# Optimization experiments

Hardware: AMD Instinct MI355X
Metric: run time of the kernel (lower is better)

The kernel has to match this reference:

```python
import jax, jax.numpy as jnp
import numpy as np


def setup_inputs() -> dict:
    key = jax.random.key(0)
    kq, kk, kv = jax.random.split(key, 3)
    B, H, S, D = 2, 16, 2048, 64
    q = jax.random.normal(kq, (B, H, S, D), dtype=jnp.float32)
    k = jax.random.normal(kk, (B, H, S, D), dtype=jnp.float32)
    v = jax.random.normal(kv, (B, H, S, D), dtype=jnp.float32)
    return {"q": q, "k": k, "v": v}


def reference(q, k, v):
    # Tiled attention without online softmax computes the same math as
    # standard scaled dot-product attention (non-causal).
    D = q.shape[-1]
    scale = 1.0 / jnp.sqrt(jnp.asarray(D, dtype=q.dtype))
    # scores: [B, H, Sq, Sk]
    scores = jnp.einsum("bhqd,bhkd->bhqk", q, k) * scale
    attn = jax.nn.softmax(scores, axis=-1)
    out = jnp.einsum("bhqk,bhkd->bhqd", attn, v)
    return out
```

## Files before the change

### kernel.cpp

```cpp
#include <hip/hip_runtime.h>
#include <hip/hip_bf16.h>


#define B_ 2
#define H_ 16
#define S_ 2048
#define D_ 64
#define BH_ (B_ * H_)
#define QBLK 128
#define KVBLK 64
#define NKV (S_ / KVBLK)
#define NWAVE 8

typedef __bf16 bf16_t;
typedef bf16_t bf16x8 __attribute__((ext_vector_type(8)));
typedef bf16_t bf16x4 __attribute__((ext_vector_type(4)));
typedef float f32x4 __attribute__((ext_vector_type(4)));

__device__ __forceinline__ f32x4 mfma_16x16x32(bf16x8 a, bf16x8 b, f32x4 c) {
  return __builtin_amdgcn_mfma_f32_16x16x32_bf16(a, b, c, 0, 0, 0);
}

__device__ __forceinline__ void gload_lds16(const bf16_t* g, bf16_t* l) {
  __builtin_amdgcn_global_load_lds(
      (const __attribute__((address_space(1))) unsigned int*)g,
      (__attribute__((address_space(3))) unsigned int*)l, 16, 0, 0);
}

__global__ void convert_k_kernel(const float* __restrict__ k, bf16_t* __restrict__ kb) {
  int i = blockIdx.x * blockDim.x + threadIdx.x;
  float4 x = ((const float4*)k)[i];
  bf16x4 o = { (bf16_t)x.x, (bf16_t)x.y, (bf16_t)x.z, (bf16_t)x.w };
  *(bf16x4*)(kb + (size_t)i * 4) = o;
}

__global__ void transpose_v_kernel(const float* __restrict__ v, bf16_t* __restrict__ vt) {
  __shared__ float tile[64][65];
  int bh = blockIdx.y, kt = blockIdx.x;
  const float* vp = v + ((size_t)bh * S_ + (size_t)kt * 64) * D_;
  int r0 = threadIdx.x >> 4;
  int c4 = (threadIdx.x & 15) * 4;
#pragma unroll
  for (int p = 0; p < 4; ++p) {
    int r = r0 + p * 16;
    float4 x = *(const float4*)(vp + (size_t)r * D_ + c4);
    tile[r][c4 + 0] = x.x; tile[r][c4 + 1] = x.y;
    tile[r][c4 + 2] = x.z; tile[r][c4 + 3] = x.w;
  }
  __syncthreads();
  bf16_t* op = vt + (size_t)bh * D_ * S_ + (size_t)kt * 64;
#pragma unroll
  for (int p = 0; p < 4; ++p) {
    int d = r0 + p * 16;
    bf16x4 o = { (bf16_t)tile[c4 + 0][d], (bf16_t)tile[c4 + 1][d],
                 (bf16_t)tile[c4 + 2][d], (bf16_t)tile[c4 + 3][d] };
    *(bf16x4*)(op + (size_t)d * S_ + c4) = o;
  }
}

__global__ __launch_bounds__(512) void attn_kernel(
    const float* __restrict__ q, const bf16_t* __restrict__ kb,
    const bf16_t* __restrict__ vt, float* __restrict__ out) {
  const int bh = blockIdx.y;
  const int qt = blockIdx.x;
  const int tid = threadIdx.x;
  const int wid = tid >> 6;
  const int lane = tid & 63;
  const int lr = lane & 15;
  const int lg = lane >> 4;

  __shared__ __align__(16) bf16_t ktile[2][KVBLK * D_];
  __shared__ __align__(16) bf16_t vtile[2][D_ * KVBLK];
  __shared__ __align__(16) bf16_t plds[NWAVE][16][72];

  const float* qp = q + ((size_t)bh * S_ + (size_t)qt * QBLK + wid * 16) * D_;
  const bf16_t* kp = kb + (size_t)bh * S_ * D_;
  const bf16_t* vp = vt + (size_t)bh * D_ * S_;

  const int srow = tid >> 3;
  const int sc = (tid & 7) ^ (srow & 7);
  const int ksrc = srow * D_ + sc * 8;
  const size_t vsrc = (size_t)srow * S_ + sc * 8;
  const int ldst = wid * 512;

  const float qscale = 0.125f * 1.4426950408889634f;
  bf16x8 bq[2];
#pragma unroll
  for (int ks = 0; ks < 2; ++ks) {
    const float* p = qp + (size_t)lr * D_ + ks * 32 + lg * 8;
    float4 x0 = *(const float4*)(p);
    float4 x1 = *(const float4*)(p + 4);
    bf16x8 a;
    a[0] = (bf16_t)(x0.x * qscale); a[1] = (bf16_t)(x0.y * qscale);
    a[2] = (bf16_t)(x0.z * qscale); a[3] = (bf16_t)(x0.w * qscale);
    a[4] = (bf16_t)(x1.x * qscale); a[5] = (bf16_t)(x1.y * qscale);
    a[6] = (bf16_t)(x1.z * qscale); a[7] = (bf16_t)(x1.w * qscale);
    bq[ks] = a;
  }

  float l = 0.f;
  f32x4 o[4];
#pragma unroll
  for (int dc = 0; dc < 4; ++dc) o[dc] = (f32x4){0.f, 0.f, 0.f, 0.f};

  gload_lds16(kp + ksrc, &ktile[0][ldst]);
  gload_lds16(vp + vsrc, &vtile[0][ldst]);
  __syncthreads();

  const int swz = lr & 7;
  const int ch_a0 = (lg ^ swz) * 8;
  const int ch_a1 = ((lg + 4) ^ swz) * 8;

  int cur = 0;
  for (int kt = 0; kt < NKV; ++kt) {
    if (kt + 1 < NKV) {
      const bf16_t* kg = kp + (size_t)(kt + 1) * (KVBLK * D_);
      const bf16_t* vg = vp + (size_t)(kt + 1) * KVBLK;
      gload_lds16(kg + ksrc, &ktile[cur ^ 1][ldst]);
      gload_lds16(vg + vsrc, &vtile[cur ^ 1][ldst]);
    }

    f32x4 s[4];
#pragma unroll
    for (int sub = 0; sub < 4; ++sub) {
      const bf16_t* krow = &ktile[cur][(sub * 16 + lr) * D_];
      bf16x8 a0 = *(const bf16x8*)(krow + ch_a0);
      bf16x8 a1 = *(const bf16x8*)(krow + ch_a1);
      f32x4 acc = (f32x4){0.f, 0.f, 0.f, 0.f};
      acc = mfma_16x16x32(a0, bq[0], acc);
      acc = mfma_16x16x32(a1, bq[1], acc);
      s[sub] = acc;
    }

    float ps = 0.f;
#pragma unroll
    for (int sub = 0; sub < 4; ++sub) {
      bf16x4 pe;
#pragma unroll
      for (int r = 0; r < 4; ++r) {
        float e = __builtin_amdgcn_exp2f(s[sub][r]);
        ps += e;
        pe[r] = (bf16_t)e;
      }
      *(bf16x4*)&plds[wid][lr][sub * 16 + lg * 4] = pe;
    }
    l += ps;

    bf16x8 pb0 = *(const bf16x8*)&plds[wid][lr][lg * 8];
    bf16x8 pb1 = *(const bf16x8*)&plds[wid][lr][32 + lg * 8];

#pragma unroll
    for (int dc = 0; dc < 4; ++dc) {
      const bf16_t* vrow = &vtile[cur][(dc * 16 + lr) * KVBLK];
      bf16x8 a0 = *(const bf16x8*)(vrow + ch_a0);
      bf16x8 a1 = *(const bf16x8*)(vrow + ch_a1);
      o[dc] = mfma_16x16x32(a0, pb0, o[dc]);
      o[dc] = mfma_16x16x32(a1, pb1, o[dc]);
    }

    __syncthreads();
    cur ^= 1;
  }

  l += __shfl_xor(l, 16, 64);
  l += __shfl_xor(l, 32, 64);
  float inv = 1.f / l;
  float* op = out + ((size_t)bh * S_ + (size_t)qt * QBLK + wid * 16 + lr) * D_;
#pragma unroll
  for (int dc = 0; dc < 4; ++dc) {
    float4 w = { o[dc][0] * inv, o[dc][1] * inv, o[dc][2] * inv, o[dc][3] * inv };
    *(float4*)(op + dc * 16 + lg * 4) = w;
  }
}

extern "C" void kernel_launch(void* const* d_in, const int* in_sizes, int n_in,
                              void* d_out, int out_size, void* d_ws, size_t ws_size,
                              hipStream_t stream) {
  const float* q = (const float*)d_in[0];
  const float* k = (const float*)d_in[1];
  const float* v = (const float*)d_in[2];
  float* out = (float*)d_out;

  bf16_t* kb = (bf16_t*)d_ws;
  bf16_t* vt = kb + (size_t)BH_ * S_ * D_;

  int n4 = (BH_ * S_ * D_) / 4;
  convert_k_kernel<<<n4 / 256, 256, 0, stream>>>(k, kb);
  transpose_v_kernel<<<dim3(S_ / 64, BH_), 256, 0, stream>>>(v, vt);
  attn_kernel<<<dim3(S_ / QBLK, BH_), 512, 0, stream>>>(q, kb, vt, out);
}
```

Before: 67.49 us.

## Process two 16-row query sub-tiles per wave with 4 waves per block

The attention kernel now runs 4 waves per block instead of 8, and each wave handles 32 query rows as two 16-row halves. Every K and V fragment read from LDS feeds two MFMAs, which halves LDS read traffic per output. Each thread issues two async global-to-LDS loads per tile to make up for having fewer threads. In exchange, register pressure rises from the doubled accumulators and Q fragments, and there are fewer waves to hide latency, though the launch bounds ask for 3 blocks per CU.

Result: slower. 76.55 us (+13.4%).

```diff
diff --git a/kernel.cpp b/kernel.cpp
--- a/kernel.cpp
+++ b/kernel.cpp
@@ -10,7 +10,7 @@
 #define QBLK 128
 #define KVBLK 64
 #define NKV (S_ / KVBLK)
-#define NWAVE 8
+#define NWAVE 4
 
 typedef __bf16 bf16_t;
 typedef bf16_t bf16x8 __attribute__((ext_vector_type(8)));
@@ -58,7 +58,7 @@
   }
 }
 
-__global__ __launch_bounds__(512) void attn_kernel(
+__global__ __launch_bounds__(256, 3) void attn_kernel(
     const float* __restrict__ q, const bf16_t* __restrict__ kb,
     const bf16_t* __restrict__ vt, float* __restrict__ out) {
   const int bh = blockIdx.y;
@@ -71,40 +71,51 @@
 
   __shared__ __align__(16) bf16_t ktile[2][KVBLK * D_];
   __shared__ __align__(16) bf16_t vtile[2][D_ * KVBLK];
-  __shared__ __align__(16) bf16_t plds[NWAVE][16][72];
-
-  const float* qp = q + ((size_t)bh * S_ + (size_t)qt * QBLK + wid * 16) * D_;
+  __shared__ __align__(16) bf16_t plds[NWAVE][32][80];
+
+  const float* qp = q + ((size_t)bh * S_ + (size_t)qt * QBLK + wid * 32) * D_;
   const bf16_t* kp = kb + (size_t)bh * S_ * D_;
   const bf16_t* vp = vt + (size_t)bh * D_ * S_;
 
-  const int srow = tid >> 3;
-  const int sc = (tid & 7) ^ (srow & 7);
-  const int ksrc = srow * D_ + sc * 8;
-  const size_t vsrc = (size_t)srow * S_ + sc * 8;
-  const int ldst = wid * 512;
+  const int p0 = wid * 128 + lane;
+  const int p1 = p0 + 64;
+  const int r0 = p0 >> 3, c0 = (p0 & 7) ^ (r0 & 7);
+  const int r1 = p1 >> 3, c1 = (p1 & 7) ^ (r1 & 7);
+  const int ks0 = r0 * D_ + c0 * 8;
+  const int ks1 = r1 * D_ + c1 * 8;
+  const size_t vs0 = (size_t)r0 * S_ + c0 * 8;
+  const size_t vs1 = (size_t)r1 * S_ + c1 * 8;
+  const int ld0 = wid * 1024;
+  const int ld1 = ld0 + 512;
 
   const float qscale = 0.125f * 1.4426950408889634f;
-  bf16x8 bq[2];
-#pragma unroll
-  for (int ks = 0; ks < 2; ++ks) {
-    const float* p = qp + (size_t)lr * D_ + ks * 32 + lg * 8;
-    float4 x0 = *(const float4*)(p);
-    float4 x1 = *(const float4*)(p + 4);
-    bf16x8 a;
-    a[0] = (bf16_t)(x0.x * qscale); a[1] = (bf16_t)(x0.y * qscale);
-    a[2] = (bf16_t)(x0.z * qscale); a[3] = (bf16_t)(x0.w * qscale);
-    a[4] = (bf16_t)(x1.x * qscale); a[5] = (bf16_t)(x1.y * qscale);
-    a[6] = (bf16_t)(x1.z * qscale); a[7] = (bf16_t)(x1.w * qscale);
-    bq[ks] = a;
-  }
-
-  float l = 0.f;
-  f32x4 o[4];
-#pragma unroll
-  for (int dc = 0; dc < 4; ++dc) o[dc] = (f32x4){0.f, 0.f, 0.f, 0.f};
-
-  gload_lds16(kp + ksrc, &ktile[0][ldst]);
-  gload_lds16(vp + vsrc, &vtile[0][ldst]);
+  bf16x8 bq[2][2];
+#pragma unroll
+  for (int qh = 0; qh < 2; ++qh)
+#pragma unroll
+    for (int ks = 0; ks < 2; ++ks) {
+      const float* p = qp + (size_t)(qh * 16 + lr) * D_ + ks * 32 + lg * 8;
+      float4 x0 = *(const float4*)(p);
+      float4 x1 = *(const float4*)(p + 4);
+      bf16x8 a;
+      a[0] = (bf16_t)(x0.x * qscale); a[1] = (bf16_t)(x0.y * qscale);
+      a[2] = (bf16_t)(x0.z * qscale); a[3] = (bf16_t)(x0.w * qscale);
+      a[4] = (bf16_t)(x1.x * qscale); a[5] = (bf16_t)(x1.y * qscale);
+      a[6] = (bf16_t)(x1.z * qscale); a[7] = (bf16_t)(x1.w * qscale);
+      bq[qh][ks] = a;
+    }
+
+  float l[2] = {0.f, 0.f};
+  f32x4 o[2][4];
+#pragma unroll
+  for (int qh = 0; qh < 2; ++qh)
+#pragma unroll
+    for (int dc = 0; dc < 4; ++dc) o[qh][dc] = (f32x4){0.f, 0.f, 0.f, 0.f};
+
+  gload_lds16(kp + ks0, &ktile[0][ld0]);
+  gload_lds16(kp + ks1, &ktile[0][ld1]);
+  gload_lds16(vp + vs0, &vtile[0][ld0]);
+  gload_lds16(vp + vs1, &vtile[0][ld1]);
   __syncthreads();
 
   const int swz = lr & 7;
@@ -116,60 +127,80 @@
     if (kt + 1 < NKV) {
       const bf16_t* kg = kp + (size_t)(kt + 1) * (KVBLK * D_);
       const bf16_t* vg = vp + (size_t)(kt + 1) * KVBLK;
-      gload_lds16(kg + ksrc, &ktile[cur ^ 1][ldst]);
-      gload_lds16(vg + vsrc, &vtile[cur ^ 1][ldst]);
-    }
-
-    f32x4 s[4];
+      gload_lds16(kg + ks0, &ktile[cur ^ 1][ld0]);
+      gload_lds16(kg + ks1, &ktile[cur ^ 1][ld1]);
+      gload_lds16(vg + vs0, &vtile[cur ^ 1][ld0]);
+      gload_lds16(vg + vs1, &vtile[cur ^ 1][ld1]);
+    }
+
+    f32x4 s[2][4];
 #pragma unroll
     for (int sub = 0; sub < 4; ++sub) {
       const bf16_t* krow = &ktile[cur][(sub * 16 + lr) * D_];
       bf16x8 a0 = *(const bf16x8*)(krow + ch_a0);
       bf16x8 a1 = *(const bf16x8*)(krow + ch_a1);
-      f32x4 acc = (f32x4){0.f, 0.f, 0.f, 0.f};
-      acc = mfma_16x16x32(a0, bq[0], acc);
-      acc = mfma_16x16x32(a1, bq[1], acc);
-      s[sub] = acc;
-    }
-
-    float ps = 0.f;
-#pragma unroll
-    for (int sub = 0; sub < 4; ++sub) {
-      bf16x4 pe;
-#pragma unroll
-      for (int r = 0; r < 4; ++r) {
-        float e = __builtin_amdgcn_exp2f(s[sub][r]);
-        ps += e;
-        pe[r] = (bf16_t)e;
+#pragma unroll
+      for (int qh = 0; qh < 2; ++qh) {
+        f32x4 acc = (f32x4){0.f, 0.f, 0.f, 0.f};
+        acc = mfma_16x16x32(a0, bq[qh][0], acc);
+        acc = mfma_16x16x32(a1, bq[qh][1], acc);
+        s[qh][sub] = acc;
       }
-      *(bf16x4*)&plds[wid][lr][sub * 16 + lg * 4] = pe;
-    }
-    l += ps;
-
-    bf16x8 pb0 = *(const bf16x8*)&plds[wid][lr][lg * 8];
-    bf16x8 pb1 = *(const bf16x8*)&plds[wid][lr][32 + lg * 8];
+    }
+
+#pragma unroll
+    for (int qh = 0; qh < 2; ++qh) {
+      float ps = 0.f;
+#pragma unroll
+      for (int sub = 0; sub < 4; ++sub) {
+        bf16x4 pe;
+#pragma unroll
+        for (int r = 0; r < 4; ++r) {
+          float e = __builtin_amdgcn_exp2f(s[qh][sub][r]);
+          ps += e;
+          pe[r] = (bf16_t)e;
+        }
+        *(bf16x4*)&plds[wid][qh * 16 + lr][sub * 16 + lg * 4] = pe;
+      }
+      l[qh] += ps;
+    }
+
+    bf16x8 pb0[2], pb1[2];
+#pragma unroll
+    for (int qh = 0; qh < 2; ++qh) {
+      pb0[qh] = *(const bf16x8*)&plds[wid][qh * 16 + lr][lg * 8];
+      pb1[qh] = *(const bf16x8*)&plds[wid][qh * 16 + lr][32 + lg * 8];
+    }
 
 #pragma unroll
     for (int dc = 0; dc < 4; ++dc) {
       const bf16_t* vrow = &vtile[cur][(dc * 16 + lr) * KVBLK];
       bf16x8 a0 = *(const bf16x8*)(vrow + ch_a0);
       bf16x8 a1 = *(const bf16x8*)(vrow + ch_a1);
-      o[dc] = mfma_16x16x32(a0, pb0, o[dc]);
-      o[dc] = mfma_16x16x32(a1, pb1, o[dc]);
+#pragma unroll
+      for (int qh = 0; qh < 2; ++qh) {
+        o[qh][dc] = mfma_16x16x32(a0, pb0[qh], o[qh][dc]);
+        o[qh][dc] = mfma_16x16x32(a1, pb1[qh], o[qh][dc]);
+      }
     }
 
     __syncthreads();
     cur ^= 1;
   }
 
-  l += __shfl_xor(l, 16, 64);
-  l += __shfl_xor(l, 32, 64);
-  float inv = 1.f / l;
-  float* op = out + ((size_t)bh * S_ + (size_t)qt * QBLK + wid * 16 + lr) * D_;
-#pragma unroll
-  for (int dc = 0; dc < 4; ++dc) {
-    float4 w = { o[dc][0] * inv, o[dc][1] * inv, o[dc][2] * inv, o[dc][3] * inv };
-    *(float4*)(op + dc * 16 + lg * 4) = w;
+#pragma unroll
+  for (int qh = 0; qh < 2; ++qh) {
+    float lq = l[qh];
+    lq += __shfl_xor(lq, 16, 64);
+    lq += __shfl_xor(lq, 32, 64);
+    float inv = 1.f / lq;
+    float* op = out + ((size_t)bh * S_ + (size_t)qt * QBLK + wid * 32 + qh * 16 + lr) * D_;
+#pragma unroll
+    for (int dc = 0; dc < 4; ++dc) {
+      float4 w = { o[qh][dc][0] * inv, o[qh][dc][1] * inv,
+                   o[qh][dc][2] * inv, o[qh][dc][3] * inv };
+      *(float4*)(op + dc * 16 + lg * 4) = w;
+    }
   }
 }
 
@@ -187,5 +218,5 @@
   int n4 = (BH_ * S_ * D_) / 4;
   convert_k_kernel<<<n4 / 256, 256, 0, stream>>>(k, kb);
   transpose_v_kernel<<<dim3(S_ / 64, BH_), 256, 0, stream>>>(v, vt);
-  attn_kernel<<<dim3(S_ / QBLK, BH_), 512, 0, stream>>>(q, kb, vt, out);
-}
+  attn_kernel<<<dim3(S_ / QBLK, BH_), 256, 0, stream>>>(q, kb, vt, out);
+}
```

## Switch attention to 32x32x16 MFMA with in-register P and split-KV waves

Applied to the files above, without the earlier changes.

Rewrites the attention kernel to use 32x32x16 bf16 MFMA tiles. Each wave now owns 32 query rows and one of two KV halves, so the block processes two KV tiles per iteration and the two partial results are combined in LDS at the end. The softmax probabilities are packed to bf16 with v_cvt_pk_bf16_f32 and rearranged with v_permlane32_swap, which removes the per-iteration LDS round trip for P. The aim is fewer MFMA issues and fewer LDS accesses per unit of work. The cost is higher register pressure, a 64KB LDS footprint, and an extra cross-wave reduction.

Result: faster. 58.87 us (-12.8%).

```diff
diff --git a/kernel.cpp b/kernel.cpp
--- a/kernel.cpp
+++ b/kernel.cpp
@@ -1,5 +1,6 @@
 #include <hip/hip_runtime.h>
 #include <hip/hip_bf16.h>
+#include <stdint.h>
 
 
 #define B_ 2
@@ -10,15 +11,26 @@
 #define QBLK 128
 #define KVBLK 64
 #define NKV (S_ / KVBLK)
-#define NWAVE 8
+#define NPER (NKV / 2)
 
 typedef __bf16 bf16_t;
 typedef bf16_t bf16x8 __attribute__((ext_vector_type(8)));
 typedef bf16_t bf16x4 __attribute__((ext_vector_type(4)));
-typedef float f32x4 __attribute__((ext_vector_type(4)));
-
-__device__ __forceinline__ f32x4 mfma_16x16x32(bf16x8 a, bf16x8 b, f32x4 c) {
-  return __builtin_amdgcn_mfma_f32_16x16x32_bf16(a, b, c, 0, 0, 0);
+typedef float f32x16 __attribute__((ext_vector_type(16)));
+typedef uint32_t u32;
+
+__device__ __forceinline__ f32x16 mfma32(bf16x8 a, bf16x8 b, f32x16 c) {
+  return __builtin_amdgcn_mfma_f32_32x32x16_bf16(a, b, c, 0, 0, 0);
+}
+
+__device__ __forceinline__ u32 cvt_pk_bf16(float lo, float hi) {
+  u32 r;
+  asm("v_cvt_pk_bf16_f32 %0, %1, %2" : "=v"(r) : "v"(lo), "v"(hi));
+  return r;
+}
+
+__device__ __forceinline__ void swap32(u32& x, u32& y) {
+  asm("v_permlane32_swap_b32 %0, %1" : "+v"(x), "+v"(y));
 }
 
 __device__ __forceinline__ void gload_lds16(const bf16_t* g, bf16_t* l) {
@@ -58,7 +70,7 @@
   }
 }
 
-__global__ __launch_bounds__(512) void attn_kernel(
+__global__ __launch_bounds__(512, 4) void attn_kernel(
     const float* __restrict__ q, const bf16_t* __restrict__ kb,
     const bf16_t* __restrict__ vt, float* __restrict__ out) {
   const int bh = blockIdx.y;
@@ -66,28 +78,32 @@
   const int tid = threadIdx.x;
   const int wid = tid >> 6;
   const int lane = tid & 63;
-  const int lr = lane & 15;
-  const int lg = lane >> 4;
-
-  __shared__ __align__(16) bf16_t ktile[2][KVBLK * D_];
-  __shared__ __align__(16) bf16_t vtile[2][D_ * KVBLK];
-  __shared__ __align__(16) bf16_t plds[NWAVE][16][72];
-
-  const float* qp = q + ((size_t)bh * S_ + (size_t)qt * QBLK + wid * 16) * D_;
+  const int wq = wid & 3;
+  const int wkv = wid >> 2;
+  const int l31 = lane & 31;
+  const int hi = lane >> 5;
+
+  __shared__ __align__(16) char smem[65536];
+  bf16_t* kbuf = (bf16_t*)smem;
+  bf16_t* vbuf = (bf16_t*)(smem + 32768);
+  float* epi = (float*)smem;
+
   const bf16_t* kp = kb + (size_t)bh * S_ * D_;
   const bf16_t* vp = vt + (size_t)bh * D_ * S_;
 
   const int srow = tid >> 3;
-  const int sc = (tid & 7) ^ (srow & 7);
-  const int ksrc = srow * D_ + sc * 8;
-  const size_t vsrc = (size_t)srow * S_ + sc * 8;
+  const int scol = (tid & 7) ^ (srow & 7);
+  const int kofs = srow * D_ + scol * 8;
+  const size_t vofs = (size_t)srow * S_ + scol * 8;
   const int ldst = wid * 512;
 
   const float qscale = 0.125f * 1.4426950408889634f;
-  bf16x8 bq[2];
-#pragma unroll
-  for (int ks = 0; ks < 2; ++ks) {
-    const float* p = qp + (size_t)lr * D_ + ks * 32 + lg * 8;
+  const int qrow = qt * QBLK + wq * 32 + l31;
+  const float* qpr = q + ((size_t)bh * S_ + qrow) * D_;
+  bf16x8 bq[4];
+#pragma unroll
+  for (int ks = 0; ks < 4; ++ks) {
+    const float* p = qpr + ks * 16 + hi * 8;
     float4 x0 = *(const float4*)(p);
     float4 x1 = *(const float4*)(p + 4);
     bf16x8 a;
@@ -98,78 +114,112 @@
     bq[ks] = a;
   }
 
-  float l = 0.f;
-  f32x4 o[4];
-#pragma unroll
-  for (int dc = 0; dc < 4; ++dc) o[dc] = (f32x4){0.f, 0.f, 0.f, 0.f};
-
-  gload_lds16(kp + ksrc, &ktile[0][ldst]);
-  gload_lds16(vp + vsrc, &vtile[0][ldst]);
+  float lsum = 0.f;
+  f32x16 o0, o1;
+#pragma unroll
+  for (int r = 0; r < 16; ++r) { o0[r] = 0.f; o1[r] = 0.f; }
+
+#pragma unroll
+  for (int par = 0; par < 2; ++par) {
+    gload_lds16(kp + (size_t)par * (KVBLK * D_) + kofs, kbuf + par * 4096 + ldst);
+    gload_lds16(vp + (size_t)par * KVBLK + vofs, vbuf + par * 4096 + ldst);
+  }
   __syncthreads();
 
-  const int swz = lr & 7;
-  const int ch_a0 = (lg ^ swz) * 8;
-  const int ch_a1 = ((lg + 4) ^ swz) * 8;
-
-  int cur = 0;
-  for (int kt = 0; kt < NKV; ++kt) {
-    if (kt + 1 < NKV) {
-      const bf16_t* kg = kp + (size_t)(kt + 1) * (KVBLK * D_);
-      const bf16_t* vg = vp + (size_t)(kt + 1) * KVBLK;
-      gload_lds16(kg + ksrc, &ktile[cur ^ 1][ldst]);
-      gload_lds16(vg + vsrc, &vtile[cur ^ 1][ldst]);
+  for (int p = 0; p < NPER; ++p) {
+    if (p + 1 < NPER) {
+      const int nb = ((p + 1) & 1) * 2;
+#pragma unroll
+      for (int par = 0; par < 2; ++par) {
+        const int t = 2 * p + 2 + par;
+        gload_lds16(kp + (size_t)t * (KVBLK * D_) + kofs,
+                    kbuf + (nb + par) * 4096 + ldst);
+        gload_lds16(vp + (size_t)t * KVBLK + vofs,
+                    vbuf + (nb + par) * 4096 + ldst);
+      }
     }
 
-    f32x4 s[4];
-#pragma unroll
-    for (int sub = 0; sub < 4; ++sub) {
-      const bf16_t* krow = &ktile[cur][(sub * 16 + lr) * D_];
-      bf16x8 a0 = *(const bf16x8*)(krow + ch_a0);
-      bf16x8 a1 = *(const bf16x8*)(krow + ch_a1);
-      f32x4 acc = (f32x4){0.f, 0.f, 0.f, 0.f};
-      acc = mfma_16x16x32(a0, bq[0], acc);
-      acc = mfma_16x16x32(a1, bq[1], acc);
-      s[sub] = acc;
+    const bf16_t* kt_ = kbuf + ((p & 1) * 2 + wkv) * 4096;
+    const bf16_t* vt_ = vbuf + ((p & 1) * 2 + wkv) * 4096;
+
+    u32 w[2][8];
+#pragma unroll
+    for (int sub = 0; sub < 2; ++sub) {
+      f32x16 sv;
+#pragma unroll
+      for (int r = 0; r < 16; ++r) sv[r] = 0.f;
+#pragma unroll
+      for (int ks = 0; ks < 4; ++ks) {
+        const int row = sub * 32 + l31;
+        const int ch = (2 * ks + hi) ^ (row & 7);
+        bf16x8 a = *(const bf16x8*)(kt_ + row * D_ + ch * 8);
+        sv = mfma32(a, bq[ks], sv);
+      }
+#pragma unroll
+      for (int b = 0; b < 4; ++b) {
+        float e0 = __builtin_amdgcn_exp2f(sv[4 * b + 0]);
+        float e1 = __builtin_amdgcn_exp2f(sv[4 * b + 1]);
+        float e2 = __builtin_amdgcn_exp2f(sv[4 * b + 2]);
+        float e3 = __builtin_amdgcn_exp2f(sv[4 * b + 3]);
+        lsum += (e0 + e1) + (e2 + e3);
+        w[sub][2 * b + 0] = cvt_pk_bf16(e0, e1);
+        w[sub][2 * b + 1] = cvt_pk_bf16(e2, e3);
+      }
+#pragma unroll
+      for (int kt2 = 0; kt2 < 2; ++kt2) {
+        swap32(w[sub][4 * kt2 + 0], w[sub][4 * kt2 + 2]);
+        swap32(w[sub][4 * kt2 + 1], w[sub][4 * kt2 + 3]);
+      }
     }
 
-    float ps = 0.f;
-#pragma unroll
-    for (int sub = 0; sub < 4; ++sub) {
-      bf16x4 pe;
-#pragma unroll
-      for (int r = 0; r < 4; ++r) {
-        float e = __builtin_amdgcn_exp2f(s[sub][r]);
-        ps += e;
-        pe[r] = (bf16_t)e;
-      }
-      *(bf16x4*)&plds[wid][lr][sub * 16 + lg * 4] = pe;
+#pragma unroll
+    for (int sub = 0; sub < 2; ++sub)
+#pragma unroll
+      for (int kt2 = 0; kt2 < 2; ++kt2) {
+        union { u32 u[4]; bf16x8 v; } pb;
+        pb.u[0] = w[sub][4 * kt2 + 0]; pb.u[1] = w[sub][4 * kt2 + 1];
+        pb.u[2] = w[sub][4 * kt2 + 2]; pb.u[3] = w[sub][4 * kt2 + 3];
+        {
+          const int row = l31;
+          const int ch = (4 * sub + 2 * kt2 + hi) ^ (row & 7);
+          bf16x8 a = *(const bf16x8*)(vt_ + row * KVBLK + ch * 8);
+          o0 = mfma32(a, pb.v, o0);
+        }
+        {
+          const int row = 32 + l31;
+          const int ch = (4 * sub + 2 * kt2 + hi) ^ (row & 7);
+          bf16x8 a = *(const bf16x8*)(vt_ + row * KVBLK + ch * 8);
+          o1 = mfma32(a, pb.v, o1);
+        }
+      }
+
+    __syncthreads();
+  }
+
+  if (wkv == 1) {
+    float* e = epi + ((size_t)wq * 64 + lane) * 33;
+#pragma unroll
+    for (int r = 0; r < 16; ++r) { e[r] = o0[r]; e[16 + r] = o1[r]; }
+    e[32] = lsum;
+  }
+  __syncthreads();
+  if (wkv == 0) {
+    const float* e = epi + ((size_t)wq * 64 + lane) * 33;
+#pragma unroll
+    for (int r = 0; r < 16; ++r) { o0[r] += e[r]; o1[r] += e[16 + r]; }
+    lsum += e[32];
+    float ltot = lsum + __shfl_xor(lsum, 32, 64);
+    float inv = 1.f / ltot;
+    float* op = out + ((size_t)bh * S_ + qrow) * D_;
+#pragma unroll
+    for (int b = 0; b < 4; ++b) {
+      float4 w0 = { o0[4 * b + 0] * inv, o0[4 * b + 1] * inv,
+                    o0[4 * b + 2] * inv, o0[4 * b + 3] * inv };
+      *(float4*)(op + 8 * b + 4 * hi) = w0;
+      float4 w1 = { o1[4 * b + 0] * inv, o1[4 * b + 1] * inv,
+                    o1[4 * b + 2] * inv, o1[4 * b + 3] * inv };
+      *(float4*)(op + 32 + 8 * b + 4 * hi) = w1;
     }
-    l += ps;
-
-    bf16x8 pb0 = *(const bf16x8*)&plds[wid][lr][lg * 8];
-    bf16x8 pb1 = *(const bf16x8*)&plds[wid][lr][32 + lg * 8];
-
-#pragma unroll
-    for (int dc = 0; dc < 4; ++dc) {
-      const bf16_t* vrow = &vtile[cur][(dc * 16 + lr) * KVBLK];
-      bf16x8 a0 = *(const bf16x8*)(vrow + ch_a0);
-      bf16x8 a1 = *(const bf16x8*)(vrow + ch_a1);
-      o[dc] = mfma_16x16x32(a0, pb0, o[dc]);
-      o[dc] = mfma_16x16x32(a1, pb1, o[dc]);
-    }
-
-    __syncthreads();
-    cur ^= 1;
-  }
-
-  l += __shfl_xor(l, 16, 64);
-  l += __shfl_xor(l, 32, 64);
-  float inv = 1.f / l;
-  float* op = out + ((size_t)bh * S_ + (size_t)qt * QBLK + wid * 16 + lr) * D_;
-#pragma unroll
-  for (int dc = 0; dc < 4; ++dc) {
-    float4 w = { o[dc][0] * inv, o[dc][1] * inv, o[dc][2] * inv, o[dc][3] * inv };
-    *(float4*)(op + dc * 16 + lg * 4) = w;
   }
 }
 
```
